# Kernel optimization log

Hardware: AMD Instinct MI355X
Metric: run time of the kernel (lower is better)

The kernel has to match this reference:

```python
import jax, jax.numpy as jnp
import numpy as np

N = 1048576   # total nodes
B = 32768     # number of graphs
F = 128       # input_dim
STEPS = 6


def setup_inputs() -> dict:
    key = jax.random.key(0)
    k0, k1, k2, k3, k4 = jax.random.split(key, 5)
    s = 1.0 / np.sqrt(F)  # torch LSTM init scale
    x = jax.random.normal(k0, (N, F), dtype=jnp.float32)
    # equal-sized, sorted graph assignment so every graph is non-empty
    batch = (jnp.arange(N, dtype=jnp.int64) * B) // N
    W_ih = jax.random.uniform(k1, (4 * F, 2 * F), jnp.float32, -s, s)
    W_hh = jax.random.uniform(k2, (4 * F, F), jnp.float32, -s, s)
    b_ih = jax.random.uniform(k3, (4 * F,), jnp.float32, -s, s)
    b_hh = jax.random.uniform(k4, (4 * F,), jnp.float32, -s, s)
    return {"x": x, "batch": batch, "W_ih": W_ih, "W_hh": W_hh,
            "b_ih": b_ih, "b_hh": b_hh}


def _lstm_cell(x_in, h, c, W_ih, W_hh, b_ih, b_hh):
    # torch gate order: i, f, g, o
    gates = x_in @ W_ih.T + h @ W_hh.T + b_ih + b_hh  # [B, 4F]
    i, f, g, o = jnp.split(gates, 4, axis=-1)
    c_new = jax.nn.sigmoid(f) * c + jax.nn.sigmoid(i) * jnp.tanh(g)
    h_new = jax.nn.sigmoid(o) * jnp.tanh(c_new)
    return h_new, c_new


def reference(x, batch, W_ih, W_hh, b_ih, b_hh):
    # Vectorized set2set: each graph's batch-1 LSTM is independent, so we run
    # all B graphs' LSTMs as one batched cell, and do the softmax-attention
    # readout with segment ops over the ragged node sets.
    h = jnp.zeros((B, F), x.dtype)
    c = jnp.zeros((B, F), x.dtype)
    q_star = jnp.zeros((B, 2 * F), x.dtype)
    batch = batch.astype(jnp.int32)
    for _ in range(STEPS):
        q, c = _lstm_cell(q_star, h, c, W_ih, W_hh, b_ih, b_hh)  # [B, F]
        h = q
        e = jnp.sum(x * q[batch], axis=-1)  # [N] attention logits
        # per-graph stable softmax
        emax = jax.ops.segment_max(e, batch, num_segments=B)
        ee = jnp.exp(e - emax[batch])
        denom = jax.ops.segment_sum(ee, batch, num_segments=B)
        a = ee / denom[batch]  # [N]
        r = jax.ops.segment_sum(a[:, None] * x, batch, num_segments=B)  # [B, F]
        q_star = jnp.concatenate([q, r], axis=-1)  # [B, 2F]
    return q_star
```

## Files before the change

kernel.cpp:

```cpp
#include <hip/hip_runtime.h>
#include <hip/hip_bf16.h>
#include <hip/hip_fp16.h>
#include <cstdint>


#define NSTEPS   6
#define NSEG     32768
#define NCHUNK   32768
#define MAXC     8
#define XSH      136
#define MTHREADS 1024
#define MGRID    256
#define ESHIFT   20.0f

typedef _Float16 half2_t __attribute__((ext_vector_type(2)));

__device__ __forceinline__ float sigmoidf_(float v) {
    return 1.0f / (1.0f + __expf(-v));
}

__device__ __forceinline__ float fdot2_(unsigned int w, unsigned int q, float acc) {
    return __builtin_amdgcn_fdot2(__builtin_bit_cast(half2_t, w),
                                  __builtin_bit_cast(half2_t, q), acc, false);
}

__device__ __forceinline__ void lgkm_barrier() {
    asm volatile("s_waitcnt lgkmcnt(0)" ::: "memory");
    __builtin_amdgcn_s_barrier();
    asm volatile("" ::: "memory");
}

__global__ void pack_weights_kernel(const float* __restrict__ Wih,
                                    const float* __restrict__ Whh,
                                    const float* __restrict__ bih,
                                    const float* __restrict__ bhh,
                                    float* __restrict__ wtp,
                                    float* __restrict__ b4) {
    const int k = blockIdx.x;
    const int f = threadIdx.x;
    float w[4];
    #pragma unroll
    for (int j = 0; j < 4; ++j) {
        const int row = j * 128 + f;
        float v = Wih[row * 256 + k];
        if (k < 128) v += Whh[row * 128 + k];
        w[j] = v;
    }
    float4 wv; wv.x = w[0]; wv.y = w[1]; wv.z = w[2]; wv.w = w[3];
    reinterpret_cast<float4*>(wtp)[k * 128 + f] = wv;
    if (k == 0) {
        float4 bv;
        bv.x = bih[0 * 128 + f] + bhh[0 * 128 + f];
        bv.y = bih[1 * 128 + f] + bhh[1 * 128 + f];
        bv.z = bih[2 * 128 + f] + bhh[2 * 128 + f];
        bv.w = bih[3 * 128 + f] + bhh[3 * 128 + f];
        reinterpret_cast<float4*>(b4)[f] = bv;
    }
}

__global__ void pack_f16_kernel(const float* __restrict__ wtp,
                                uint4* __restrict__ wph) {
    const int p = blockIdx.x;
    const int f = threadIdx.x;
    const float4 w0 = reinterpret_cast<const float4*>(wtp)[(2 * p) * 128 + f];
    const float4 w1 = reinterpret_cast<const float4*>(wtp)[(2 * p + 1) * 128 + f];
    __half2 h[4];
    h[0] = __floats2half2_rn(w0.x, w1.x);
    h[1] = __floats2half2_rn(w0.y, w1.y);
    h[2] = __floats2half2_rn(w0.z, w1.z);
    h[3] = __floats2half2_rn(w0.w, w1.w);
    wph[p * 128 + f] = *reinterpret_cast<uint4*>(h);
}

__global__ void zero_kernel(int* __restrict__ p, int n) {
    for (int i = blockIdx.x * blockDim.x + threadIdx.x; i < n;
         i += gridDim.x * blockDim.x) p[i] = 0;
}

__global__ void seg_count_kernel(const int* __restrict__ batch,
                                 int* __restrict__ counts) {
    const int c = blockIdx.x * blockDim.x + threadIdx.x;
    if (c < NCHUNK) {
        const int v = batch[c * 32];
        if (v >= 0 && v < NSEG)
            atomicAdd(&counts[v], 1);
    }
}

__global__ __launch_bounds__(1024)
void scan_kernel(const int* __restrict__ counts,
                 int* __restrict__ offs, int* __restrict__ cursor,
                 int* __restrict__ activeList, int* __restrict__ nActive) {
    __shared__ int sc[1024];
    const int t = threadIdx.x;
    const int base = t * 32;
    int local[32];
    int sum = 0;
    #pragma unroll
    for (int j = 0; j < 32; ++j) { local[j] = counts[base + j]; sum += local[j]; }
    sc[t] = sum;
    __syncthreads();
    for (int d = 1; d < 1024; d <<= 1) {
        const int v = (t >= d) ? sc[t - d] : 0;
        __syncthreads();
        sc[t] += v;
        __syncthreads();
    }
    int run = sc[t] - sum;
    for (int j = 0; j < 32; ++j) {
        const int s = base + j;
        offs[s] = run;
        cursor[s] = run;
        if (local[j] > 0) {
            const int idx = atomicAdd(nActive, 1);
            activeList[idx] = s;
        }
        run += local[j];
    }
}

__global__ void fill_kernel(const int* __restrict__ batch,
                            int* __restrict__ cursor,
                            int* __restrict__ chunk_list) {
    const int c = blockIdx.x * blockDim.x + threadIdx.x;
    if (c < NCHUNK) {
        const int v = batch[c * 32];
        if (v >= 0 && v < NSEG) {
            const int pos = atomicAdd(&cursor[v], 1);
            chunk_list[pos] = c;
        }
    }
}

__global__ __launch_bounds__(128)
void empty_traj_kernel(const float* __restrict__ wtp,
                       const float* __restrict__ b4,
                       float* __restrict__ qe,
                       float* __restrict__ qe01) {
    __shared__ float q_s[128];
    const int f = threadIdx.x;
    const float4 bb = reinterpret_cast<const float4*>(b4)[f];
    q_s[f] = 0.0f;
    float c = 0.0f;
    __syncthreads();
    for (int step = 0; step < NSTEPS; ++step) {
        float a0 = 0.f, a1 = 0.f, a2 = 0.f, a3 = 0.f;
        for (int k = 0; k < 128; ++k) {
            const float4 w = reinterpret_cast<const float4*>(wtp)[k * 128 + f];
            const float qv = q_s[k];
            a0 = fmaf(w.x, qv, a0); a1 = fmaf(w.y, qv, a1);
            a2 = fmaf(w.z, qv, a2); a3 = fmaf(w.w, qv, a3);
        }
        __syncthreads();
        c = sigmoidf_(a1 + bb.y) * c + sigmoidf_(a0 + bb.x) * tanhf(a2 + bb.z);
        const float qv = sigmoidf_(a3 + bb.w) * tanhf(c);
        q_s[f] = qv;
        if (step == 0) { qe01[f] = qv; qe01[128 + f] = c; }
        __syncthreads();
    }
    qe[f] = q_s[f];
}

__global__ void bcast_empty_kernel(const int* __restrict__ counts,
                                   const float* __restrict__ qe,
                                   float* __restrict__ out) {
    const int lane = threadIdx.x & 63;
    const int wave0 = (blockIdx.x * blockDim.x + threadIdx.x) >> 6;
    const int nwave = (gridDim.x * blockDim.x) >> 6;
    float4 v = make_float4(0.f, 0.f, 0.f, 0.f);
    if (lane < 32) v = reinterpret_cast<const float4*>(qe)[lane];
    for (int s = wave0; s < NSEG; s += nwave) {
        if (counts[s] != 0) continue;
        reinterpret_cast<float4*>(out)[(size_t)s * 64 + lane] = v;
    }
}

#define GATE_STEP(WA, WB, M)                                                 \
    {                                                                        \
        const uint2 qp0 =                                                    \
            *reinterpret_cast<const uint2*>(&qh0[(M) * 32 + ko * 4]);        \
        const uint2 qp1 =                                                    \
            *reinterpret_cast<const uint2*>(&qh1[(M) * 32 + ko * 4]);        \
        a00 = fdot2_((WA).x, qp0.x, a00); a01 = fdot2_((WA).y, qp0.x, a01);  \
        a02 = fdot2_((WA).z, qp0.x, a02); a03 = fdot2_((WA).w, qp0.x, a03);  \
        a00 = fdot2_((WB).x, qp0.y, a00); a01 = fdot2_((WB).y, qp0.y, a01);  \
        a02 = fdot2_((WB).z, qp0.y, a02); a03 = fdot2_((WB).w, qp0.y, a03);  \
        a10 = fdot2_((WA).x, qp1.x, a10); a11 = fdot2_((WA).y, qp1.x, a11);  \
        a12 = fdot2_((WA).z, qp1.x, a12); a13 = fdot2_((WA).w, qp1.x, a13);  \
        a10 = fdot2_((WB).x, qp1.y, a10); a11 = fdot2_((WB).y, qp1.y, a11);  \
        a12 = fdot2_((WB).z, qp1.y, a12); a13 = fdot2_((WB).w, qp1.y, a13);  \
    }

__global__ __launch_bounds__(MTHREADS, 4)
__attribute__((amdgpu_waves_per_eu(4, 4)))
void main_seg_kernel(const float* __restrict__ x,
                     const uint4* __restrict__ wph,
                     const float* __restrict__ b4,
                     const float* __restrict__ qe01,
                     const int* __restrict__ counts,
                     const int* __restrict__ offs,
                     const int* __restrict__ chunk_list,
                     const int* __restrict__ activeList,
                     const int* __restrict__ nActive,
                     float* __restrict__ out) {
    __shared__ __align__(16) __half x_h[2][256][XSH];
    __shared__ __align__(16) __half q_h[2][2][256];
    __shared__ __align__(16) float  e_s[2][256];
    __shared__ __align__(16) float  rpart_s[2][8][128];
    __shared__ float dsum_s[16];
    __shared__ int   clist_s[2][MAXC];
    __shared__ int   cnt_s[2];

    const int t  = threadIdx.x;
    const int ko = t & 7;
    const int f  = t >> 3;
    const float4 bb = reinterpret_cast<const float4*>(b4)[f];
    const float c0v = qe01[128 + f];
    const int nAct  = *nActive;
    const int nPair = (nAct + 1) >> 1;

    const uint4 W0a = wph[(0 * 16 + ko * 2 + 0) * 128 + f];
    const uint4 W0b = wph[(0 * 16 + ko * 2 + 1) * 128 + f];
    const uint4 W1a = wph[(1 * 16 + ko * 2 + 0) * 128 + f];
    const uint4 W1b = wph[(1 * 16 + ko * 2 + 1) * 128 + f];
    const uint4 W2a = wph[(2 * 16 + ko * 2 + 0) * 128 + f];
    const uint4 W2b = wph[(2 * 16 + ko * 2 + 1) * 128 + f];
    const uint4 W3a = wph[(3 * 16 + ko * 2 + 0) * 128 + f];
    const uint4 W3b = wph[(3 * 16 + ko * 2 + 1) * 128 + f];
    const uint4 W4a = wph[(4 * 16 + ko * 2 + 0) * 128 + f];
    const uint4 W4b = wph[(4 * 16 + ko * 2 + 1) * 128 + f];
    const uint4 W5a = wph[(5 * 16 + ko * 2 + 0) * 128 + f];
    const uint4 W5b = wph[(5 * 16 + ko * 2 + 1) * 128 + f];
    const uint4 W6a = wph[(6 * 16 + ko * 2 + 0) * 128 + f];
    const uint4 W6b = wph[(6 * 16 + ko * 2 + 1) * 128 + f];
    const uint4 W7a = wph[(7 * 16 + ko * 2 + 0) * 128 + f];
    const uint4 W7b = wph[(7 * 16 + ko * 2 + 1) * 128 + f];

    const int we  = t >> 6, le = t & 63;
    const int sgE = we >> 3, nE = (we & 7) * 32 + (le >> 1), khE = le & 1;
    const int gR = le >> 4, iR = le & 15;

    for (int pp = blockIdx.x; pp < nPair; pp += gridDim.x) {
        if (t < 2) {
            const int idx = 2 * pp + t;
            int cnt = 0;
            if (idx < nAct) {
                const int sseg = activeList[idx];
                cnt = counts[sseg];
                if (cnt > MAXC) cnt = MAXC;
                const int off = offs[sseg];
                for (int j = 0; j < cnt; ++j) clist_s[t][j] = chunk_list[off + j];
                for (int a = 1; a < cnt; ++a) {
                    const int key = clist_s[t][a];
                    int b = a - 1;
                    while (b >= 0 && clist_s[t][b] > key) {
                        clist_s[t][b + 1] = clist_s[t][b]; --b;
                    }
                    clist_s[t][b + 1] = key;
                }
            }
            cnt_s[t] = cnt;
        }
        if (t < 256) q_h[0][t >> 7][t & 127] = __float2half(qe01[t & 127]);
        __syncthreads();
        const int cnt0 = cnt_s[0], cnt1 = cnt_s[1];
        const int nvE = ((sgE == 0) ? cnt0 : cnt1) * 32;

        #pragma unroll
        for (int sg = 0; sg < 2; ++sg) {
            const int cnt = (sg == 0) ? cnt0 : cnt1;
            for (int p = t; p < cnt * 1024; p += MTHREADS) {
                const int j = p >> 10, g = p & 1023;
                const int row = g >> 5, c4 = g & 31;
                const float4 v = reinterpret_cast<const float4*>(x)
                                    [(size_t)clist_s[sg][j] * 1024 + g];
                __half2* dst =
                    reinterpret_cast<__half2*>(&x_h[sg][j * 32 + row][c4 * 4]);
                dst[0] = __floats2half2_rn(v.x, v.y);
                dst[1] = __floats2half2_rn(v.z, v.w);
            }
            if (cnt < MAXC) {
                const int base = cnt * 32;
                const int nh2 = (256 - base) * (XSH / 2);
                for (int p = t; p < nh2; p += MTHREADS) {
                    const int row = base + p / (XSH / 2);
                    const int cc  = p % (XSH / 2);
                    reinterpret_cast<__half2*>(&x_h[sg][row][0])[cc] =
                        __floats2half2_rn(0.f, 0.f);
                }
            }
        }
        float creg0 = c0v, creg1 = c0v;
        __syncthreads();

        for (int s = 0; s < NSTEPS; ++s) {
            const int cur = s & 1, prev = cur ^ 1;

            if (s > 0) {
                float a00 = 0.f, a01 = 0.f, a02 = 0.f, a03 = 0.f;
                float a10 = 0.f, a11 = 0.f, a12 = 0.f, a13 = 0.f;
                const __half* qh0 = &q_h[prev][0][0];
                const __half* qh1 = &q_h[prev][1][0];
                GATE_STEP(W0a, W0b, 0)
                GATE_STEP(W1a, W1b, 1)
                GATE_STEP(W2a, W2b, 2)
                GATE_STEP(W3a, W3b, 3)
                GATE_STEP(W4a, W4b, 4)
                GATE_STEP(W5a, W5b, 5)
                GATE_STEP(W6a, W6b, 6)
                GATE_STEP(W7a, W7b, 7)
                a00 += __shfl_xor(a00,1); a00 += __shfl_xor(a00,2); a00 += __shfl_xor(a00,4);
                a01 += __shfl_xor(a01,1); a01 += __shfl_xor(a01,2); a01 += __shfl_xor(a01,4);
                a02 += __shfl_xor(a02,1); a02 += __shfl_xor(a02,2); a02 += __shfl_xor(a02,4);
                a03 += __shfl_xor(a03,1); a03 += __shfl_xor(a03,2); a03 += __shfl_xor(a03,4);
                a10 += __shfl_xor(a10,1); a10 += __shfl_xor(a10,2); a10 += __shfl_xor(a10,4);
                a11 += __shfl_xor(a11,1); a11 += __shfl_xor(a11,2); a11 += __shfl_xor(a11,4);
                a12 += __shfl_xor(a12,1); a12 += __shfl_xor(a12,2); a12 += __shfl_xor(a12,4);
                a13 += __shfl_xor(a13,1); a13 += __shfl_xor(a13,2); a13 += __shfl_xor(a13,4);
                if (ko == 0) {
                    {
                        const float gi = a00 + bb.x, gf = a01 + bb.y;
                        const float gg = a02 + bb.z, go = a03 + bb.w;
                        creg0 = sigmoidf_(gf) * creg0 + sigmoidf_(gi) * tanhf(gg);
                        q_h[cur][0][f] = __float2half(sigmoidf_(go) * tanhf(creg0));
                    }
                    {
                        const float gi = a10 + bb.x, gf = a11 + bb.y;
                        const float gg = a12 + bb.z, go = a13 + bb.w;
                        creg1 = sigmoidf_(gf) * creg1 + sigmoidf_(gi) * tanhf(gg);
                        q_h[cur][1][f] = __float2half(sigmoidf_(go) * tanhf(creg1));
                    }
                }
                lgkm_barrier();
            }

            {
                const uint4* xr =
                    reinterpret_cast<const uint4*>(&x_h[sgE][nE][khE * 64]);
                const uint4* qr =
                    reinterpret_cast<const uint4*>(&q_h[cur][sgE][khE * 64]);
                float part = 0.f;
                #pragma unroll
                for (int kk = 0; kk < 8; ++kk) {
                    const uint4 xv = xr[kk];
                    const uint4 qv = qr[kk];
                    part = fdot2_(xv.x, qv.x, part);
                    part = fdot2_(xv.y, qv.y, part);
                    part = fdot2_(xv.z, qv.z, part);
                    part = fdot2_(xv.w, qv.w, part);
                }
                part += __shfl_xor(part, 1);
                const float p = (nE < nvE) ? __expf(part - ESHIFT) : 0.f;
                if (khE == 0) e_s[sgE][nE] = p;
                float ws = (khE == 0) ? p : 0.f;
                ws += __shfl_xor(ws, 2);  ws += __shfl_xor(ws, 4);
                ws += __shfl_xor(ws, 8);  ws += __shfl_xor(ws, 16);
                ws += __shfl_xor(ws, 32);
                if (le == 0) dsum_s[we] = ws;
                const int nlo = (we & 7) * 32;
                float r0=0.f,r1=0.f,r2=0.f,r3=0.f,r4=0.f,r5=0.f,r6=0.f,r7=0.f;
                #pragma unroll
                for (int j = 0; j < 8; ++j) {
                    const int node = nlo + j * 4 + gR;
                    const float pj = e_s[sgE][node];
                    const uint4 xv =
                        *reinterpret_cast<const uint4*>(&x_h[sgE][node][iR * 8]);
                    const float2 f0 = __half22float2(__builtin_bit_cast(__half2, xv.x));
                    const float2 f1 = __half22float2(__builtin_bit_cast(__half2, xv.y));
                    const float2 f2 = __half22float2(__builtin_bit_cast(__half2, xv.z));
                    const float2 f3 = __half22float2(__builtin_bit_cast(__half2, xv.w));
                    r0 = fmaf(pj, f0.x, r0); r1 = fmaf(pj, f0.y, r1);
                    r2 = fmaf(pj, f1.x, r2); r3 = fmaf(pj, f1.y, r3);
                    r4 = fmaf(pj, f2.x, r4); r5 = fmaf(pj, f2.y, r5);
                    r6 = fmaf(pj, f3.x, r6); r7 = fmaf(pj, f3.y, r7);
                }
                r0 += __shfl_xor(r0,16); r0 += __shfl_xor(r0,32);
                r1 += __shfl_xor(r1,16); r1 += __shfl_xor(r1,32);
                r2 += __shfl_xor(r2,16); r2 += __shfl_xor(r2,32);
                r3 += __shfl_xor(r3,16); r3 += __shfl_xor(r3,32);
                r4 += __shfl_xor(r4,16); r4 += __shfl_xor(r4,32);
                r5 += __shfl_xor(r5,16); r5 += __shfl_xor(r5,32);
                r6 += __shfl_xor(r6,16); r6 += __shfl_xor(r6,32);
                r7 += __shfl_xor(r7,16); r7 += __shfl_xor(r7,32);
                if (le < 16) {
                    float4 v0; v0.x=r0; v0.y=r1; v0.z=r2; v0.w=r3;
                    float4 v1; v1.x=r4; v1.y=r5; v1.z=r6; v1.w=r7;
                    *reinterpret_cast<float4*>(&rpart_s[sgE][we & 7][iR * 8])     = v0;
                    *reinterpret_cast<float4*>(&rpart_s[sgE][we & 7][iR * 8 + 4]) = v1;
                }
            }
            lgkm_barrier();

            if (t < 256) {
                const int sg = t >> 7, fr = t & 127;
                float den = 0.f;
                #pragma unroll
                for (int j = 0; j < 8; ++j) den += dsum_s[sg * 8 + j];
                float rsum = 0.f;
                #pragma unroll
                for (int j = 0; j < 8; ++j) rsum += rpart_s[sg][j][fr];
                q_h[cur][sg][128 + fr] = __float2half(rsum / den);
            }
            lgkm_barrier();
        }

        if (t < 512) {
            const int sg = t >> 8, i = t & 255;
            const int idx = 2 * pp + sg;
            if (idx < nAct) {
                const int sseg = activeList[idx];
                out[(size_t)sseg * 256 + i] = __half2float(q_h[1][sg][i]);
            }
        }
        __syncthreads();
    }
}

extern "C" void kernel_launch(void* const* d_in, const int* in_sizes, int n_in,
                              void* d_out, int out_size, void* d_ws, size_t ws_size,
                              hipStream_t stream) {
    (void)in_sizes; (void)n_in; (void)out_size; (void)ws_size;
    const float* x    = (const float*)d_in[0];
    const int*   batch = (const int*)d_in[1];
    const float* Wih  = (const float*)d_in[2];
    const float* Whh  = (const float*)d_in[3];
    const float* bih  = (const float*)d_in[4];
    const float* bhh  = (const float*)d_in[5];
    float* out = (float*)d_out;

    float* wtp       = (float*)d_ws;
    float* b4        = wtp + 131072;
    float* qe        = b4 + 512;
    float* qe01      = qe + 128;
    uint4* wph       = (uint4*)(qe01 + 256);
    int*   counts    = (int*)(wph + 128 * 128);
    int*   offs      = counts + NSEG;
    int*   cursor    = offs + NSEG;
    int*   chunk_lst = cursor + NSEG;
    int*   activeLst = chunk_lst + NCHUNK;
    int*   nActive   = activeLst + NSEG;

    pack_weights_kernel<<<256, 128, 0, stream>>>(Wih, Whh, bih, bhh, wtp, b4);
    pack_f16_kernel<<<128, 128, 0, stream>>>(wtp, wph);
    zero_kernel<<<64, 256, 0, stream>>>(counts, NSEG);
    zero_kernel<<<1, 64, 0, stream>>>(nActive, 1);
    seg_count_kernel<<<NCHUNK / 256, 256, 0, stream>>>(batch, counts);
    scan_kernel<<<1, 1024, 0, stream>>>(counts, offs, cursor, activeLst, nActive);
    fill_kernel<<<NCHUNK / 256, 256, 0, stream>>>(batch, cursor, chunk_lst);
    empty_traj_kernel<<<1, 128, 0, stream>>>(wtp, b4, qe, qe01);
    bcast_empty_kernel<<<512, 256, 0, stream>>>(counts, qe, out);
    main_seg_kernel<<<MGRID, MTHREADS, 0, stream>>>(
        x, wph, b4, qe01, counts, offs, chunk_lst, activeLst, nActive, out);
}
```

Baseline: 323.7 us.

## Stagger two segments' LSTM and attention phases to overlap across barriers

Instead of processing both segments in lockstep, with the whole block split in halves for attention, the block now handles one segment at a time with all 1024 threads. Each segment's gate computation or r-finalize is interleaved with the other segment's attention phase so they share barrier intervals. Attention work per thread halves (4 nodes per thread, 4-way k split), and the partial reduction now spans 16 waves. This changes the barrier count and ordering and adds more reduction partials per segment. Gate FLOPs are unchanged.

```diff
diff --git a/kernel.cpp b/kernel.cpp
--- a/kernel.cpp
+++ b/kernel.cpp
@@ -175,21 +175,94 @@
     }
 }
 
-#define GATE_STEP(WA, WB, M)                                                 \
+#define GATE1(QH, WA, WB, M)                                                 \
     {                                                                        \
-        const uint2 qp0 =                                                    \
-            *reinterpret_cast<const uint2*>(&qh0[(M) * 32 + ko * 4]);        \
-        const uint2 qp1 =                                                    \
-            *reinterpret_cast<const uint2*>(&qh1[(M) * 32 + ko * 4]);        \
-        a00 = fdot2_((WA).x, qp0.x, a00); a01 = fdot2_((WA).y, qp0.x, a01);  \
-        a02 = fdot2_((WA).z, qp0.x, a02); a03 = fdot2_((WA).w, qp0.x, a03);  \
-        a00 = fdot2_((WB).x, qp0.y, a00); a01 = fdot2_((WB).y, qp0.y, a01);  \
-        a02 = fdot2_((WB).z, qp0.y, a02); a03 = fdot2_((WB).w, qp0.y, a03);  \
-        a10 = fdot2_((WA).x, qp1.x, a10); a11 = fdot2_((WA).y, qp1.x, a11);  \
-        a12 = fdot2_((WA).z, qp1.x, a12); a13 = fdot2_((WA).w, qp1.x, a13);  \
-        a10 = fdot2_((WB).x, qp1.y, a10); a11 = fdot2_((WB).y, qp1.y, a11);  \
-        a12 = fdot2_((WB).z, qp1.y, a12); a13 = fdot2_((WB).w, qp1.y, a13);  \
-    }
+        const uint2 qp =                                                     \
+            *reinterpret_cast<const uint2*>(&(QH)[(M) * 32 + ko * 4]);       \
+        a0 = fdot2_((WA).x, qp.x, a0); a1 = fdot2_((WA).y, qp.x, a1);        \
+        a2 = fdot2_((WA).z, qp.x, a2); a3 = fdot2_((WA).w, qp.x, a3);        \
+        a0 = fdot2_((WB).x, qp.y, a0); a1 = fdot2_((WB).y, qp.y, a1);        \
+        a2 = fdot2_((WB).z, qp.y, a2); a3 = fdot2_((WB).w, qp.y, a3);        \
+    }
+
+#define GATE_SEG(QH, CREG, QOUT) do {                                        \
+    float a0 = 0.f, a1 = 0.f, a2 = 0.f, a3 = 0.f;                            \
+    GATE1(QH, W0a, W0b, 0) GATE1(QH, W1a, W1b, 1)                            \
+    GATE1(QH, W2a, W2b, 2) GATE1(QH, W3a, W3b, 3)                            \
+    GATE1(QH, W4a, W4b, 4) GATE1(QH, W5a, W5b, 5)                            \
+    GATE1(QH, W6a, W6b, 6) GATE1(QH, W7a, W7b, 7)                            \
+    a0 += __shfl_xor(a0, 1); a0 += __shfl_xor(a0, 2); a0 += __shfl_xor(a0, 4); \
+    a1 += __shfl_xor(a1, 1); a1 += __shfl_xor(a1, 2); a1 += __shfl_xor(a1, 4); \
+    a2 += __shfl_xor(a2, 1); a2 += __shfl_xor(a2, 2); a2 += __shfl_xor(a2, 4); \
+    a3 += __shfl_xor(a3, 1); a3 += __shfl_xor(a3, 2); a3 += __shfl_xor(a3, 4); \
+    if (ko == 0) {                                                           \
+        const float gi = a0 + bb.x, gf = a1 + bb.y;                          \
+        const float gg = a2 + bb.z, go = a3 + bb.w;                          \
+        CREG = sigmoidf_(gf) * (CREG) + sigmoidf_(gi) * tanhf(gg);           \
+        (QOUT)[f] = __float2half(sigmoidf_(go) * tanhf(CREG));               \
+    }                                                                        \
+} while (0)
+
+#define E_RP_SEG(SG, BUF, NV) do {                                           \
+    const uint4* xr = reinterpret_cast<const uint4*>(&x_h[SG][nE][khE * 32]); \
+    const uint4* qr = reinterpret_cast<const uint4*>(&q_h[BUF][SG][khE * 32]); \
+    float part = 0.f;                                                        \
+    _Pragma("unroll")                                                        \
+    for (int kk = 0; kk < 4; ++kk) {                                         \
+        const uint4 xv = xr[kk]; const uint4 qv = qr[kk];                    \
+        part = fdot2_(xv.x, qv.x, part); part = fdot2_(xv.y, qv.y, part);    \
+        part = fdot2_(xv.z, qv.z, part); part = fdot2_(xv.w, qv.w, part);    \
+    }                                                                        \
+    part += __shfl_xor(part, 1); part += __shfl_xor(part, 2);                \
+    const float p = (nE < (NV)) ? __expf(part - ESHIFT) : 0.f;               \
+    if (khE == 0) e_s[SG][nE] = p;                                           \
+    float ws = (khE == 0) ? p : 0.f;                                         \
+    ws += __shfl_xor(ws, 4);  ws += __shfl_xor(ws, 8);                       \
+    ws += __shfl_xor(ws, 16); ws += __shfl_xor(ws, 32);                      \
+    if (le == 0) dsum_s[SG][we] = ws;                                        \
+    float r0=0.f,r1=0.f,r2=0.f,r3=0.f,r4=0.f,r5=0.f,r6=0.f,r7=0.f;           \
+    _Pragma("unroll")                                                        \
+    for (int j = 0; j < 4; ++j) {                                            \
+        const int node = (we << 4) + j * 4 + gR;                             \
+        const float pj = e_s[SG][node];                 \
+        const uint4 xv =                                                     \
+            *reinterpret_cast<const uint4*>(&x_h[SG][node][iR * 8]);         \
+        const float2 f0 = __half22float2(__builtin_bit_cast(__half2, xv.x)); \
+        const float2 f1 = __half22float2(__builtin_bit_cast(__half2, xv.y)); \
+        const float2 f2 = __half22float2(__builtin_bit_cast(__half2, xv.z)); \
+        const float2 f3 = __half22float2(__builtin_bit_cast(__half2, xv.w)); \
+        r0 = fmaf(pj, f0.x, r0); r1 = fmaf(pj, f0.y, r1);                    \
+        r2 = fmaf(pj, f1.x, r2); r3 = fmaf(pj, f1.y, r3);                    \
+        r4 = fmaf(pj, f2.x, r4); r5 = fmaf(pj, f2.y, r5);                    \
+        r6 = fmaf(pj, f3.x, r6); r7 = fmaf(pj, f3.y, r7);                    \
+    }                                                                        \
+    r0 += __shfl_xor(r0, 16); r0 += __shfl_xor(r0, 32);                      \
+    r1 += __shfl_xor(r1, 16); r1 += __shfl_xor(r1, 32);                      \
+    r2 += __shfl_xor(r2, 16); r2 += __shfl_xor(r2, 32);                      \
+    r3 += __shfl_xor(r3, 16); r3 += __shfl_xor(r3, 32);                      \
+    r4 += __shfl_xor(r4, 16); r4 += __shfl_xor(r4, 32);                      \
+    r5 += __shfl_xor(r5, 16); r5 += __shfl_xor(r5, 32);                      \
+    r6 += __shfl_xor(r6, 16); r6 += __shfl_xor(r6, 32);                      \
+    r7 += __shfl_xor(r7, 16); r7 += __shfl_xor(r7, 32);                      \
+    if (le < 16) {                                                           \
+        float4 v0; v0.x=r0; v0.y=r1; v0.z=r2; v0.w=r3;                       \
+        float4 v1; v1.x=r4; v1.y=r5; v1.z=r6; v1.w=r7;                       \
+        *reinterpret_cast<float4*>(&rpart_s[SG][we][iR * 8])     = v0;       \
+        *reinterpret_cast<float4*>(&rpart_s[SG][we][iR * 8 + 4]) = v1;       \
+    }                                                                        \
+} while (0)
+
+#define RFIN_SEG(SG, BUF) do {                                               \
+    if (t < 128) {                                                           \
+        float den = 0.f;                                                     \
+        _Pragma("unroll")                                                    \
+        for (int w2 = 0; w2 < 16; ++w2) den += dsum_s[SG][w2];               \
+        float rsum = 0.f;                                                    \
+        _Pragma("unroll")                                                    \
+        for (int w2 = 0; w2 < 16; ++w2) rsum += rpart_s[SG][w2][t];          \
+        q_h[BUF][SG][128 + t] = __float2half(rsum / den);                    \
+    }                                                                        \
+} while (0)
 
 __global__ __launch_bounds__(MTHREADS, 4)
 __attribute__((amdgpu_waves_per_eu(4, 4)))
@@ -206,8 +279,8 @@
     __shared__ __align__(16) __half x_h[2][256][XSH];
     __shared__ __align__(16) __half q_h[2][2][256];
     __shared__ __align__(16) float  e_s[2][256];
-    __shared__ __align__(16) float  rpart_s[2][8][128];
-    __shared__ float dsum_s[16];
+    __shared__ __align__(16) float  rpart_s[2][16][128];
+    __shared__ float dsum_s[2][16];
     __shared__ int   clist_s[2][MAXC];
     __shared__ int   cnt_s[2];
 
@@ -237,8 +310,8 @@
     const uint4 W7b = wph[(7 * 16 + ko * 2 + 1) * 128 + f];
 
     const int we  = t >> 6, le = t & 63;
-    const int sgE = we >> 3, nE = (we & 7) * 32 + (le >> 1), khE = le & 1;
-    const int gR = le >> 4, iR = le & 15;
+    const int nE  = t >> 2, khE = t & 3;
+    const int gR  = le >> 4, iR = le & 15;
 
     for (int pp = blockIdx.x; pp < nPair; pp += gridDim.x) {
         if (t < 2) {
@@ -264,7 +337,7 @@
         if (t < 256) q_h[0][t >> 7][t & 127] = __float2half(qe01[t & 127]);
         __syncthreads();
         const int cnt0 = cnt_s[0], cnt1 = cnt_s[1];
-        const int nvE = ((sgE == 0) ? cnt0 : cnt1) * 32;
+        const int nv0 = cnt0 * 32, nv1 = cnt1 * 32;
 
         #pragma unroll
         for (int sg = 0; sg < 2; ++sg) {
@@ -294,115 +367,23 @@
         __syncthreads();
 
         for (int s = 0; s < NSTEPS; ++s) {
-            const int cur = s & 1, prev = cur ^ 1;
+            const int bc = s & 1;
+            const int bp = bc ^ 1;
 
             if (s > 0) {
-                float a00 = 0.f, a01 = 0.f, a02 = 0.f, a03 = 0.f;
-                float a10 = 0.f, a11 = 0.f, a12 = 0.f, a13 = 0.f;
-                const __half* qh0 = &q_h[prev][0][0];
-                const __half* qh1 = &q_h[prev][1][0];
-                GATE_STEP(W0a, W0b, 0)
-                GATE_STEP(W1a, W1b, 1)
-                GATE_STEP(W2a, W2b, 2)
-                GATE_STEP(W3a, W3b, 3)
-                GATE_STEP(W4a, W4b, 4)
-                GATE_STEP(W5a, W5b, 5)
-                GATE_STEP(W6a, W6b, 6)
-                GATE_STEP(W7a, W7b, 7)
-                a00 += __shfl_xor(a00,1); a00 += __shfl_xor(a00,2); a00 += __shfl_xor(a00,4);
-                a01 += __shfl_xor(a01,1); a01 += __shfl_xor(a01,2); a01 += __shfl_xor(a01,4);
-                a02 += __shfl_xor(a02,1); a02 += __shfl_xor(a02,2); a02 += __shfl_xor(a02,4);
-                a03 += __shfl_xor(a03,1); a03 += __shfl_xor(a03,2); a03 += __shfl_xor(a03,4);
-                a10 += __shfl_xor(a10,1); a10 += __shfl_xor(a10,2); a10 += __shfl_xor(a10,4);
-                a11 += __shfl_xor(a11,1); a11 += __shfl_xor(a11,2); a11 += __shfl_xor(a11,4);
-                a12 += __shfl_xor(a12,1); a12 += __shfl_xor(a12,2); a12 += __shfl_xor(a12,4);
-                a13 += __shfl_xor(a13,1); a13 += __shfl_xor(a13,2); a13 += __shfl_xor(a13,4);
-                if (ko == 0) {
-                    {
-                        const float gi = a00 + bb.x, gf = a01 + bb.y;
-                        const float gg = a02 + bb.z, go = a03 + bb.w;
-                        creg0 = sigmoidf_(gf) * creg0 + sigmoidf_(gi) * tanhf(gg);
-                        q_h[cur][0][f] = __float2half(sigmoidf_(go) * tanhf(creg0));
-                    }
-                    {
-                        const float gi = a10 + bb.x, gf = a11 + bb.y;
-                        const float gg = a12 + bb.z, go = a13 + bb.w;
-                        creg1 = sigmoidf_(gf) * creg1 + sigmoidf_(gi) * tanhf(gg);
-                        q_h[cur][1][f] = __float2half(sigmoidf_(go) * tanhf(creg1));
-                    }
-                }
+                GATE_SEG((&q_h[bp][0][0]), creg0, (&q_h[bc][0][0]));
+                RFIN_SEG(1, bp);
                 lgkm_barrier();
+                GATE_SEG((&q_h[bp][1][0]), creg1, (&q_h[bc][1][0]));
             }
-
-            {
-                const uint4* xr =
-                    reinterpret_cast<const uint4*>(&x_h[sgE][nE][khE * 64]);
-                const uint4* qr =
-                    reinterpret_cast<const uint4*>(&q_h[cur][sgE][khE * 64]);
-                float part = 0.f;
-                #pragma unroll
-                for (int kk = 0; kk < 8; ++kk) {
-                    const uint4 xv = xr[kk];
-                    const uint4 qv = qr[kk];
-                    part = fdot2_(xv.x, qv.x, part);
-                    part = fdot2_(xv.y, qv.y, part);
-                    part = fdot2_(xv.z, qv.z, part);
-                    part = fdot2_(xv.w, qv.w, part);
-                }
-                part += __shfl_xor(part, 1);
-                const float p = (nE < nvE) ? __expf(part - ESHIFT) : 0.f;
-                if (khE == 0) e_s[sgE][nE] = p;
-                float ws = (khE == 0) ? p : 0.f;
-                ws += __shfl_xor(ws, 2);  ws += __shfl_xor(ws, 4);
-                ws += __shfl_xor(ws, 8);  ws += __shfl_xor(ws, 16);
-                ws += __shfl_xor(ws, 32);
-                if (le == 0) dsum_s[we] = ws;
-                const int nlo = (we & 7) * 32;
-                float r0=0.f,r1=0.f,r2=0.f,r3=0.f,r4=0.f,r5=0.f,r6=0.f,r7=0.f;
-                #pragma unroll
-                for (int j = 0; j < 8; ++j) {
-                    const int node = nlo + j * 4 + gR;
-                    const float pj = e_s[sgE][node];
-                    const uint4 xv =
-                        *reinterpret_cast<const uint4*>(&x_h[sgE][node][iR * 8]);
-                    const float2 f0 = __half22float2(__builtin_bit_cast(__half2, xv.x));
-                    const float2 f1 = __half22float2(__builtin_bit_cast(__half2, xv.y));
-                    const float2 f2 = __half22float2(__builtin_bit_cast(__half2, xv.z));
-                    const float2 f3 = __half22float2(__builtin_bit_cast(__half2, xv.w));
-                    r0 = fmaf(pj, f0.x, r0); r1 = fmaf(pj, f0.y, r1);
-                    r2 = fmaf(pj, f1.x, r2); r3 = fmaf(pj, f1.y, r3);
-                    r4 = fmaf(pj, f2.x, r4); r5 = fmaf(pj, f2.y, r5);
-                    r6 = fmaf(pj, f3.x, r6); r7 = fmaf(pj, f3.y, r7);
-                }
-                r0 += __shfl_xor(r0,16); r0 += __shfl_xor(r0,32);
-                r1 += __shfl_xor(r1,16); r1 += __shfl_xor(r1,32);
-                r2 += __shfl_xor(r2,16); r2 += __shfl_xor(r2,32);
-                r3 += __shfl_xor(r3,16); r3 += __shfl_xor(r3,32);
-                r4 += __shfl_xor(r4,16); r4 += __shfl_xor(r4,32);
-                r5 += __shfl_xor(r5,16); r5 += __shfl_xor(r5,32);
-                r6 += __shfl_xor(r6,16); r6 += __shfl_xor(r6,32);
-                r7 += __shfl_xor(r7,16); r7 += __shfl_xor(r7,32);
-                if (le < 16) {
-                    float4 v0; v0.x=r0; v0.y=r1; v0.z=r2; v0.w=r3;
-                    float4 v1; v1.x=r4; v1.y=r5; v1.z=r6; v1.w=r7;
-                    *reinterpret_cast<float4*>(&rpart_s[sgE][we & 7][iR * 8])     = v0;
-                    *reinterpret_cast<float4*>(&rpart_s[sgE][we & 7][iR * 8 + 4]) = v1;
-                }
-            }
+            E_RP_SEG(0, bc, nv0);
             lgkm_barrier();
-
-            if (t < 256) {
-                const int sg = t >> 7, fr = t & 127;
-                float den = 0.f;
-                #pragma unroll
-                for (int j = 0; j < 8; ++j) den += dsum_s[sg * 8 + j];
-                float rsum = 0.f;
-                #pragma unroll
-                for (int j = 0; j < 8; ++j) rsum += rpart_s[sg][j][fr];
-                q_h[cur][sg][128 + fr] = __float2half(rsum / den);
-            }
+            RFIN_SEG(0, bc);
+            E_RP_SEG(1, bc, nv1);
             lgkm_barrier();
         }
+        RFIN_SEG(1, 1);
+        lgkm_barrier();
 
         if (t < 512) {
             const int sg = t >> 8, i = t & 255;
```

Result: slower. 347.6 us (+7.4%).
